# Optimization experiments

Measured on AMD Instinct MI355X. Metric: run time of the kernel, lower is better.

Reference implementation:

```python
import jax, jax.numpy as jnp
import numpy as np

B, T, C, H = 4, 2048, 1024, 16
D = C // H  # head_dim = 64


def setup_inputs() -> dict:
    key = jax.random.key(0)
    ks = jax.random.split(key, 5)
    scale = 0.02
    return {
        "x": jax.random.normal(ks[0], (B, T, C), dtype=jnp.float32),
        "w_qkv": jax.random.normal(ks[1], (C, 3 * C), dtype=jnp.float32) * scale,
        "b_qkv": jnp.zeros((3 * C,), dtype=jnp.float32),
        "w_out": jax.random.normal(ks[2], (C, C), dtype=jnp.float32) * scale,
        "b_out": jnp.zeros((C,), dtype=jnp.float32),
    }


def reference(x, w_qkv, b_qkv, w_out, b_out):
    Bx, Tx, Cx = x.shape
    qkv = x @ w_qkv + b_qkv  # [B,T,3C]
    q, k, v = jnp.split(qkv, 3, axis=-1)
    # [B,T,C] -> [B,H,T,D]
    def heads(t):
        return t.reshape(Bx, Tx, H, D).transpose(0, 2, 1, 3)
    q, k, v = heads(q), heads(k), heads(v)
    scores = jnp.einsum("bhtd,bhsd->bhts", q, k) / jnp.sqrt(jnp.float32(D))
    causal = jnp.tril(jnp.ones((Tx, Tx), dtype=bool))
    scores = jnp.where(causal[None, None], scores, -jnp.inf)
    attn = jax.nn.softmax(scores, axis=-1)
    y = jnp.einsum("bhts,bhsd->bhtd", attn, v)  # [B,H,T,D]
    y = y.transpose(0, 2, 1, 3).reshape(Bx, Tx, Cx)
    return y @ w_out + b_out
```

## Files before the change

### kernel.cpp

```cpp
#include <hip/hip_runtime.h>
#include <hip/hip_bf16.h>
#include <math.h>

typedef __bf16 bf16;
typedef __bf16 bf16x8 __attribute__((ext_vector_type(8)));
typedef __bf16 bf16x4 __attribute__((ext_vector_type(4)));
typedef float  f32x4  __attribute__((ext_vector_type(4)));

__device__ __forceinline__ void gld_lds16(const bf16* g, bf16* l) {
    void* gv = (void*)g;
    __builtin_amdgcn_global_load_lds(
        (__attribute__((address_space(1))) void*)gv,
        (__attribute__((address_space(3))) void*)l, 16, 0, 0);
}

__global__ void k_cvt_bf16(const float* __restrict__ in, bf16* __restrict__ out, int n4) {
    int i = blockIdx.x * blockDim.x + threadIdx.x;
    if (i < n4) {
        float4 v = ((const float4*)in)[i];
        bf16x4 o;
        o[0] = (bf16)v.x; o[1] = (bf16)v.y; o[2] = (bf16)v.z; o[3] = (bf16)v.w;
        ((bf16x4*)out)[i] = o;
    }
}

__global__ void k_transpose_cvt(const float* __restrict__ in, bf16* __restrict__ out,
                                int R, int C) {
    __shared__ float tile[64][68];
    int c0 = blockIdx.x * 64, r0 = blockIdx.y * 64;
    int tid = threadIdx.x;
#pragma unroll
    for (int i = 0; i < 4; ++i) {
        int chunk = tid + i * 256;
        int r = chunk >> 4, c4 = (chunk & 15) * 4;
        float4 v = *(const float4*)(in + (size_t)(r0 + r) * C + c0 + c4);
        tile[r][c4 + 0] = v.x; tile[r][c4 + 1] = v.y;
        tile[r][c4 + 2] = v.z; tile[r][c4 + 3] = v.w;
    }
    __syncthreads();
#pragma unroll
    for (int i = 0; i < 2; ++i) {
        int chunk = tid + i * 256;
        int c = chunk >> 3, k8 = (chunk & 7) * 8;
        bf16x8 v;
#pragma unroll
        for (int j = 0; j < 8; ++j) v[j] = (bf16)tile[k8 + j][c];
        *(bf16x8*)(out + (size_t)(c0 + c) * R + r0 + k8) = v;
    }
}

__global__ void k_transpose_v(const bf16* __restrict__ qkv, bf16* __restrict__ vt) {
    __shared__ bf16 tile[64][72];
    int bh = blockIdx.y, b = bh >> 4, h = bh & 15;
    int t0 = blockIdx.x * 64;
    int tid = threadIdx.x;
    const bf16* src = qkv + (size_t)(b * 2048 + t0) * 3072 + 2048 + h * 64;
#pragma unroll
    for (int i = 0; i < 2; ++i) {
        int chunk = tid + i * 256;
        int t = chunk >> 3, d8 = (chunk & 7) * 8;
        bf16x8 v = *(const bf16x8*)(src + (size_t)t * 3072 + d8);
#pragma unroll
        for (int j = 0; j < 8; ++j) tile[t][d8 + j] = v[j];
    }
    __syncthreads();
#pragma unroll
    for (int i = 0; i < 2; ++i) {
        int chunk = tid + i * 256;
        int d = chunk >> 3, t8 = (chunk & 7) * 8;
        bf16x8 v;
#pragma unroll
        for (int j = 0; j < 8; ++j) v[j] = tile[t8 + j][d];
        *(bf16x8*)(vt + ((size_t)bh * 64 + d) * 2048 + t0 + t8) = v;
    }
}

template <bool OUT_BF16>
__global__ __launch_bounds__(256, 2) void k_gemm(
    const bf16* __restrict__ A, const bf16* __restrict__ Bt,
    const float* __restrict__ bias, void* __restrict__ Cout,
    int M, int N, int K) {
    __shared__ __align__(16) bf16 lA[2][4096];
    __shared__ __align__(16) bf16 lB[2][4096];
    int tid = threadIdx.x;
    int wid = tid >> 6, lane = tid & 63;
    int quad = lane >> 4, l16 = lane & 15;
    int bm = blockIdx.y * 128, bn = blockIdx.x * 128;
    int wm = (wid >> 1) * 64, wn = (wid & 1) * 64;

    f32x4 zero = {0.f, 0.f, 0.f, 0.f};
    f32x4 acc[4][4];
#pragma unroll
    for (int i = 0; i < 4; ++i)
#pragma unroll
        for (int j = 0; j < 4; ++j) acc[i][j] = zero;

    for (int k0 = 0; k0 < K; k0 += 64) {
        __syncthreads();
#pragma unroll
        for (int i = 0; i < 4; ++i) {
            int j = (wid * 4 + i) * 64 + lane;
            int kf = j >> 9, row = (j & 511) >> 2, c8 = (j & 3) * 8;
            gld_lds16(A  + (size_t)(bm + row) * K + k0 + kf * 32 + c8, &lA[0][0] + (wid * 4 + i) * 512);
            gld_lds16(Bt + (size_t)(bn + row) * K + k0 + kf * 32 + c8, &lB[0][0] + (wid * 4 + i) * 512);
        }
        __syncthreads();
#pragma unroll
        for (int kk = 0; kk < 2; ++kk) {
            bf16x8 af[4], bg[4];
#pragma unroll
            for (int i = 0; i < 4; ++i) {
                af[i] = *(const bf16x8*)(&lA[kk][(wm + i * 16 + l16) * 32 + quad * 8]);
                bg[i] = *(const bf16x8*)(&lB[kk][(wn + i * 16 + l16) * 32 + quad * 8]);
            }
#pragma unroll
            for (int i = 0; i < 4; ++i)
#pragma unroll
                for (int j = 0; j < 4; ++j)
                    acc[i][j] = __builtin_amdgcn_mfma_f32_16x16x32_bf16(af[i], bg[j], acc[i][j], 0, 0, 0);
        }
    }
#pragma unroll
    for (int i = 0; i < 4; ++i) {
#pragma unroll
        for (int j = 0; j < 4; ++j) {
            int col = bn + wn + j * 16 + l16;
            float bv = bias ? bias[col] : 0.f;
#pragma unroll
            for (int r = 0; r < 4; ++r) {
                int row = bm + wm + i * 16 + quad * 4 + r;
                float v = acc[i][j][r] + bv;
                if (OUT_BF16) ((bf16*)Cout)[(size_t)row * N + col] = (bf16)v;
                else          ((float*)Cout)[(size_t)row * N + col] = v;
            }
        }
    }
}

__global__ __launch_bounds__(256, 3) void k_attn(
    const bf16* __restrict__ qkv,
    const bf16* __restrict__ vt,
    bf16* __restrict__ y) {
    __shared__ __align__(16) bf16 lK[2][4096];
    __shared__ __align__(16) bf16 lV[2][4096];
    __shared__ __align__(16) bf16 lP[4][32 * 72];

    const int T = 2048, CQ = 3072;
    int tid = threadIdx.x, wid = tid >> 6, lane = tid & 63;
    int quad = lane >> 4, l16 = lane & 15;
    int x = blockIdx.x;
    int bh = ((x & 7) << 3) | ((x >> 3) & 7);
    int qb = 15 - (x >> 6);
    int b = bh >> 4, h = bh & 15;
    int q0 = qb * 128;
    int rb = qb * 4 + wid;
    int mdiag = rb >> 1;
    int ntiles = qb * 2 + 2;

    const bf16* qbase = qkv + (size_t)(b * T + q0 + wid * 32) * CQ + h * 64;
    const bf16* kbase = qkv + (size_t)(b * T) * CQ + 1024 + h * 64;
    const bf16* vbase = vt + (size_t)bh * 64 * T;
    bf16* lPw = lP[wid];

    auto stage = [&](int kt, int buf) {
        int t0 = kt * 64;
#pragma unroll
        for (int i = 0; i < 2; ++i) {
            int j = (wid * 2 + i) * 64 + lane;
            int kf = j >> 8, r = (j & 255) >> 2, c8 = (j & 3) * 8;
            gld_lds16(kbase + (size_t)(t0 + r) * CQ + kf * 32 + c8, &lK[buf][(wid * 2 + i) * 512]);
            gld_lds16(vbase + (size_t)r * T + t0 + kf * 32 + c8,    &lV[buf][(wid * 2 + i) * 512]);
        }
    };

    bf16x8 qf[2][2];
#pragma unroll
    for (int qi = 0; qi < 2; ++qi)
#pragma unroll
        for (int kf = 0; kf < 2; ++kf) {
            bf16x8 v = *(const bf16x8*)(qbase + (size_t)(qi * 16 + l16) * CQ + kf * 32 + quad * 8);
#pragma unroll
            for (int j = 0; j < 8; ++j) v[j] = (bf16)((float)v[j] * 0.125f);
            qf[qi][kf] = v;
        }

    f32x4 zero = {0.f, 0.f, 0.f, 0.f};
    f32x4 m10 = {-10.f, -10.f, -10.f, -10.f};
    f32x4 o[2][4];
    float lsum[2] = {0.f, 0.f};
#pragma unroll
    for (int qi = 0; qi < 2; ++qi)
#pragma unroll
        for (int i = 0; i < 4; ++i) o[qi][i] = zero;

    stage(0, 0);
    for (int kt = 0; kt < ntiles; ++kt) {
        __syncthreads();
        if (kt + 1 < ntiles) stage(kt + 1, (kt + 1) & 1);
        if (kt > mdiag) continue;
        const bf16* Kb = lK[kt & 1];
        const bf16* Vb = lV[kt & 1];
        bool diag = (kt == mdiag);
        bool half = diag && !(rb & 1);
        int in_hi = half ? 2 : 4;

        f32x4 s[2][4];
#pragma unroll
        for (int qi = 0; qi < 2; ++qi)
#pragma unroll
            for (int in = 0; in < 4; ++in) s[qi][in] = m10;
        for (int kf = 0; kf < 2; ++kf)
            for (int in = 0; in < in_hi; ++in) {
                bf16x8 kb = *(const bf16x8*)(Kb + kf * 2048 + (in * 16 + l16) * 32 + quad * 8);
#pragma unroll
                for (int qi = 0; qi < 2; ++qi)
                    s[qi][in] = __builtin_amdgcn_mfma_f32_16x16x32_bf16(kb, qf[qi][kf], s[qi][in], 0, 0, 0);
            }

        bf16x8 vb[2][4];
#pragma unroll
        for (int kf = 0; kf < 2; ++kf)
#pragma unroll
            for (int dn = 0; dn < 4; ++dn)
                vb[kf][dn] = *(const bf16x8*)(Vb + kf * 2048 + (dn * 16 + l16) * 32 + quad * 8);

        int rl0 = (rb * 32) - kt * 64;
        for (int qi = 0; qi < 2; ++qi) {
            int qloc = rl0 + qi * 16 + l16;
#pragma unroll
            for (int in = 0; in < 4; ++in) {
                bf16x4 pk4;
                if (in >= in_hi) {
                    pk4[0] = pk4[1] = pk4[2] = pk4[3] = (bf16)0.f;
                } else {
#pragma unroll
                    for (int r = 0; r < 4; ++r) {
                        float e = __expf(s[qi][in][r]);
                        if (diag) {
                            int tloc = in * 16 + quad * 4 + r;
                            if (tloc > qloc) e = 0.f;
                        }
                        lsum[qi] += e;
                        pk4[r] = (bf16)e;
                    }
                }
                *(bf16x4*)(lPw + (qi * 16 + l16) * 72 + in * 16 + quad * 4) = pk4;
            }
        }

#pragma unroll
        for (int qi = 0; qi < 2; ++qi)
#pragma unroll
            for (int kf = 0; kf < 2; ++kf) {
                bf16x8 pa = *(const bf16x8*)(lPw + (qi * 16 + l16) * 72 + kf * 32 + quad * 8);
#pragma unroll
                for (int dn = 0; dn < 4; ++dn)
                    o[qi][dn] = __builtin_amdgcn_mfma_f32_16x16x32_bf16(pa, vb[kf][dn], o[qi][dn], 0, 0, 0);
            }
    }

    float linv[2];
#pragma unroll
    for (int qi = 0; qi < 2; ++qi) {
        float l = lsum[qi];
        l += __shfl_xor(l, 16, 64);
        l += __shfl_xor(l, 32, 64);
        linv[qi] = 1.f / l;
    }
#pragma unroll
    for (int qi = 0; qi < 2; ++qi)
#pragma unroll
        for (int r = 0; r < 4; ++r) {
            float li = __shfl(linv[qi], quad * 4 + r, 64);
            int row = q0 + wid * 32 + qi * 16 + quad * 4 + r;
#pragma unroll
            for (int dn = 0; dn < 4; ++dn) {
                float v = o[qi][dn][r] * li;
                y[(size_t)(b * T + row) * 1024 + h * 64 + dn * 16 + l16] = (bf16)v;
            }
        }
}

extern "C" void kernel_launch(void* const* d_in, const int* in_sizes, int n_in,
                              void* d_out, int out_size, void* d_ws, size_t ws_size,
                              hipStream_t stream) {
    const float* x     = (const float*)d_in[0];
    const float* w_qkv = (const float*)d_in[1];
    const float* b_qkv = (const float*)d_in[2];
    const float* w_out = (const float*)d_in[3];
    const float* b_out = (const float*)d_in[4];
    float* out = (float*)d_out;

    const int B = 4, T = 2048, C = 1024, H = 16;
    const int M = B * T;

    char* ws = (char*)d_ws;
    bf16* xb    = (bf16*)(ws);
    bf16* wqkvT = (bf16*)(ws + (16ull << 20));
    bf16* woutT = (bf16*)(ws + (22ull << 20));
    bf16* qkvb  = (bf16*)(ws + (24ull << 20));
    bf16* yb    = (bf16*)(ws + (72ull << 20));
    bf16* vtb   = xb;

    k_cvt_bf16<<<(M * C / 4 + 255) / 256, 256, 0, stream>>>(x, xb, M * C / 4);
    k_transpose_cvt<<<dim3(3 * C / 64, C / 64), 256, 0, stream>>>(w_qkv, wqkvT, C, 3 * C);
    k_transpose_cvt<<<dim3(C / 64, C / 64), 256, 0, stream>>>(w_out, woutT, C, C);
    k_gemm<true><<<dim3(3 * C / 128, M / 128), 256, 0, stream>>>(xb, wqkvT, b_qkv, qkvb, M, 3 * C, C);
    k_transpose_v<<<dim3(T / 64, B * H), 256, 0, stream>>>(qkvb, vtb);
    k_attn<<<dim3(1024, 1), 256, 0, stream>>>(qkvb, vtb, yb);
    k_gemm<false><<<dim3(C / 128, M / 128), 256, 0, stream>>>(yb, woutT, b_out, out, M, C, C);
}
```

Measured before the change: 281.1 us.

## Use exp2 softmax, MFMA row sums, swizzled P buffer, higher occupancy

Folds log2(e) into the Q scale so exp2f replaces __expf, and drops the constant -10 score offset. The per-row softmax denominator is now computed by an extra MFMA of P against a ones vector, which removes the scalar accumulation and the cross-lane shuffles at the end. The P staging buffer shrinks to 16x64 per wave with an XOR swizzle, reused per qi. Launch bounds go from 3 to 4 blocks per CU. In exchange this adds MFMA work, and removing the offset could risk overflow for large scores.

```diff
diff --git a/kernel.cpp b/kernel.cpp
--- a/kernel.cpp
+++ b/kernel.cpp
@@ -137,15 +137,16 @@
     }
 }
 
-__global__ __launch_bounds__(256, 3) void k_attn(
+__global__ __launch_bounds__(256, 4) void k_attn(
     const bf16* __restrict__ qkv,
     const bf16* __restrict__ vt,
     bf16* __restrict__ y) {
     __shared__ __align__(16) bf16 lK[2][4096];
     __shared__ __align__(16) bf16 lV[2][4096];
-    __shared__ __align__(16) bf16 lP[4][32 * 72];
+    __shared__ __align__(16) bf16 lP[4][1024];
 
     const int T = 2048, CQ = 3072;
+    const float QSCALE = 0.125f * 1.44269504088896f;
     int tid = threadIdx.x, wid = tid >> 6, lane = tid & 63;
     int quad = lane >> 4, l16 = lane & 15;
     int x = blockIdx.x;
@@ -180,18 +181,22 @@
         for (int kf = 0; kf < 2; ++kf) {
             bf16x8 v = *(const bf16x8*)(qbase + (size_t)(qi * 16 + l16) * CQ + kf * 32 + quad * 8);
 #pragma unroll
-            for (int j = 0; j < 8; ++j) v[j] = (bf16)((float)v[j] * 0.125f);
+            for (int j = 0; j < 8; ++j) v[j] = (bf16)((float)v[j] * QSCALE);
             qf[qi][kf] = v;
         }
 
+    bf16x8 ones;
+#pragma unroll
+    for (int j = 0; j < 8; ++j) ones[j] = (bf16)1.0f;
+
     f32x4 zero = {0.f, 0.f, 0.f, 0.f};
-    f32x4 m10 = {-10.f, -10.f, -10.f, -10.f};
-    f32x4 o[2][4];
-    float lsum[2] = {0.f, 0.f};
-#pragma unroll
-    for (int qi = 0; qi < 2; ++qi)
+    f32x4 o[2][4], o1[2];
+#pragma unroll
+    for (int qi = 0; qi < 2; ++qi) {
+        o1[qi] = zero;
 #pragma unroll
         for (int i = 0; i < 4; ++i) o[qi][i] = zero;
+    }
 
     stage(0, 0);
     for (int kt = 0; kt < ntiles; ++kt) {
@@ -208,7 +213,7 @@
 #pragma unroll
         for (int qi = 0; qi < 2; ++qi)
 #pragma unroll
-            for (int in = 0; in < 4; ++in) s[qi][in] = m10;
+            for (int in = 0; in < 4; ++in) s[qi][in] = zero;
         for (int kf = 0; kf < 2; ++kf)
             for (int in = 0; in < in_hi; ++in) {
                 bf16x8 kb = *(const bf16x8*)(Kb + kf * 2048 + (in * 16 + l16) * 32 + quad * 8);
@@ -225,6 +230,8 @@
                 vb[kf][dn] = *(const bf16x8*)(Vb + kf * 2048 + (dn * 16 + l16) * 32 + quad * 8);
 
         int rl0 = (rb * 32) - kt * 64;
+        int sw = (l16 & 7);
+#pragma unroll
         for (int qi = 0; qi < 2; ++qi) {
             int qloc = rl0 + qi * 16 + l16;
 #pragma unroll
@@ -235,43 +242,34 @@
                 } else {
 #pragma unroll
                     for (int r = 0; r < 4; ++r) {
-                        float e = __expf(s[qi][in][r]);
+                        float e = exp2f(s[qi][in][r]);
                         if (diag) {
                             int tloc = in * 16 + quad * 4 + r;
                             if (tloc > qloc) e = 0.f;
                         }
-                        lsum[qi] += e;
                         pk4[r] = (bf16)e;
                     }
                 }
-                *(bf16x4*)(lPw + (qi * 16 + l16) * 72 + in * 16 + quad * 4) = pk4;
-            }
-        }
-
-#pragma unroll
-        for (int qi = 0; qi < 2; ++qi)
+                int tb = in * 2 + (quad >> 1);
+                *(bf16x4*)(lPw + l16 * 64 + ((tb ^ sw) << 3) + (quad & 1) * 4) = pk4;
+            }
 #pragma unroll
             for (int kf = 0; kf < 2; ++kf) {
-                bf16x8 pa = *(const bf16x8*)(lPw + (qi * 16 + l16) * 72 + kf * 32 + quad * 8);
+                int tbr = kf * 4 + quad;
+                bf16x8 pa = *(const bf16x8*)(lPw + l16 * 64 + ((tbr ^ sw) << 3));
+                o1[qi] = __builtin_amdgcn_mfma_f32_16x16x32_bf16(pa, ones, o1[qi], 0, 0, 0);
 #pragma unroll
                 for (int dn = 0; dn < 4; ++dn)
                     o[qi][dn] = __builtin_amdgcn_mfma_f32_16x16x32_bf16(pa, vb[kf][dn], o[qi][dn], 0, 0, 0);
             }
-    }
-
-    float linv[2];
-#pragma unroll
-    for (int qi = 0; qi < 2; ++qi) {
-        float l = lsum[qi];
-        l += __shfl_xor(l, 16, 64);
-        l += __shfl_xor(l, 32, 64);
-        linv[qi] = 1.f / l;
-    }
+        }
+    }
+
 #pragma unroll
     for (int qi = 0; qi < 2; ++qi)
 #pragma unroll
         for (int r = 0; r < 4; ++r) {
-            float li = __shfl(linv[qi], quad * 4 + r, 64);
+            float li = 1.f / o1[qi][r];
             int row = q0 + wid * 32 + qi * 16 + quad * 4 + r;
 #pragma unroll
             for (int dn = 0; dn < 4; ++dn) {
```

New measurement: 347.3 us. 1.24x slower.
